# Performance work log

Measured on AMD Instinct MI355X. Metric: run time of the kernel, lower is better.

The kernel has to match this reference:

```python
import math
import jax, jax.numpy as jnp
import numpy as np

B, T, D = 4, 2048, 768
NH, DH = 12, 64

def setup_inputs() -> dict:
    key = jax.random.key(0)
    k1, k2, k3 = jax.random.split(key, 3)
    scale_attn = 1.0 / math.sqrt(D)
    scale_proj = 1.0 / math.sqrt(D)
    return {
        "x": jax.random.normal(k1, (B, T, D), dtype=jnp.float32),
        "w_attn": jax.random.normal(k2, (D, 3 * D), dtype=jnp.float32) * scale_attn,
        "b_attn": jnp.zeros((3 * D,), dtype=jnp.float32),
        "w_proj": jax.random.normal(k3, (D, D), dtype=jnp.float32) * scale_proj,
        "b_proj": jnp.zeros((D,), dtype=jnp.float32),
    }

def reference(x, w_attn, b_attn, w_proj, b_proj):
    Bx, Tx, Dx = x.shape
    qkv = x @ w_attn + b_attn                     # [B, T, 3D]
    q, k, v = jnp.split(qkv, 3, axis=-1)          # each [B, T, D]
    # [B, T, D] -> [B, NH, T, DH]
    def to_heads(t):
        return t.reshape(Bx, Tx, NH, DH).transpose(0, 2, 1, 3)
    q, k, v = to_heads(q), to_heads(k), to_heads(v)
    attn = jnp.einsum("bhqd,bhkd->bhqk", q, k) / math.sqrt(DH)
    causal = jnp.tril(jnp.ones((Tx, Tx), dtype=bool))
    attn = jnp.where(causal[None, None, :, :], attn, -jnp.inf)
    attn = jax.nn.softmax(attn, axis=-1)
    out = jnp.einsum("bhqk,bhkd->bhqd", attn, v)  # [B, NH, T, DH]
    out = out.transpose(0, 2, 1, 3).reshape(Bx, Tx, Dx)
    out = out @ w_proj + b_proj
    return (out, (k, v))
```

## Files before the change

### kernel.cpp

```cpp
#include <hip/hip_runtime.h>
#include <hip/hip_bf16.h>

typedef unsigned short ushort_t;
typedef __attribute__((ext_vector_type(8))) short short8;
typedef __attribute__((ext_vector_type(4))) float f32x4;

#define B_    4
#define T_    2048
#define D_    768
#define NH_   12
#define DH_   64
#define KDIM  768

__device__ __forceinline__ ushort_t f2bf(float f) {
  union { float f; unsigned u; } c; c.f = f;
  unsigned u = c.u;
  return (ushort_t)((u + 0x7FFFu + ((u >> 16) & 1u)) >> 16);
}

__device__ __forceinline__ unsigned cvt_pk_bf16(float lo, float hi) {
  unsigned r;
  asm("v_cvt_pk_bf16_f32 %0, %1, %2" : "=v"(r) : "v"(lo), "v"(hi));
  return r;
}

__device__ __forceinline__ void gload_lds16(const void* g, void* l) {
  __builtin_amdgcn_global_load_lds(
      (const __attribute__((address_space(1))) unsigned int*)g,
      (__attribute__((address_space(3))) unsigned int*)l, 16, 0, 0);
}

__global__ void cvt_bf16_vec(const float* __restrict__ in,
                             ushort_t* __restrict__ out, int n4) {
  int i = blockIdx.x * blockDim.x + threadIdx.x;
  if (i >= n4) return;
  float4 v = ((const float4*)in)[i];
  ushort4 o;
  o.x = f2bf(v.x); o.y = f2bf(v.y); o.z = f2bf(v.z); o.w = f2bf(v.w);
  ((ushort4*)out)[i] = o;
}

__global__ void transpose_cvt(const float* __restrict__ in,
                              ushort_t* __restrict__ out, int R, int C) {
  __shared__ float tile[32][33];
  int c0 = blockIdx.x * 32, r0 = blockIdx.y * 32;
  int tx = threadIdx.x, ty = threadIdx.y;
#pragma unroll
  for (int j = 0; j < 32; j += 8)
    tile[ty + j][tx] = in[(size_t)(r0 + ty + j) * C + c0 + tx];
  __syncthreads();
#pragma unroll
  for (int j = 0; j < 32; j += 8)
    out[(size_t)(c0 + ty + j) * R + r0 + tx] = f2bf(tile[tx][ty + j]);
}

__device__ __forceinline__ void gemm128_mainloop(
    const ushort_t* __restrict__ A, const ushort_t* __restrict__ BT,
    int m0, int n0, ushort_t* lds, f32x4 acc[4][4]) {
  const int t = threadIdx.x;
  const int l = t & 63;
  const int w = t >> 6;
  const int wm = w >> 1, wn = w & 1;
  const int g = l >> 4, qi = l & 15;
  const int c0 = t, c1 = t + 256;
  const int r0 = c0 >> 2, r1 = c1 >> 2;
  const int s0 = (c0 & 3) ^ ((r0 >> 2) & 3);
  const int s1 = (c1 & 3) ^ ((r1 >> 2) & 3);
  const ushort_t* ga0 = A + (size_t)(m0 + r0) * KDIM + (s0 << 3);
  const ushort_t* ga1 = A + (size_t)(m0 + r1) * KDIM + (s1 << 3);
  const ushort_t* gb0 = BT + (size_t)(n0 + r0) * KDIM + (s0 << 3);
  const ushort_t* gb1 = BT + (size_t)(n0 + r1) * KDIM + (s1 << 3);
  const int NK = KDIM / 32;
  const int rsw = (g ^ qi >> 2) << 3;

#pragma unroll
  for (int p = 0; p < 2; ++p) {
    ushort_t* lp = lds + p * 8192;
    int k0 = p * 32;
    gload_lds16(ga0 + k0, lp + w * 512);
    gload_lds16(ga1 + k0, lp + 2048 + w * 512);
    gload_lds16(gb0 + k0, lp + 4096 + w * 512);
    gload_lds16(gb1 + k0, lp + 6144 + w * 512);
  }

  int kb = 0;
  for (int kk = 0; kk < NK; ++kk) {
    if (kk < NK - 1) {
      asm volatile("s_waitcnt vmcnt(4)" ::: "memory");
    } else {
      asm volatile("s_waitcnt vmcnt(0)" ::: "memory");
    }
    __builtin_amdgcn_sched_barrier(0);
    __builtin_amdgcn_s_barrier();
    __builtin_amdgcn_sched_barrier(0);
    if (kk + 2 < NK) {
      int kb2 = kb + 2 >= 3 ? kb - 1 : kb + 2;
      ushort_t* lp = lds + kb2 * 8192;
      int k0 = (kk + 2) * 32;
      gload_lds16(ga0 + k0, lp + w * 512);
      gload_lds16(ga1 + k0, lp + 2048 + w * 512);
      gload_lds16(gb0 + k0, lp + 4096 + w * 512);
      gload_lds16(gb1 + k0, lp + 6144 + w * 512);
    }
    ushort_t* lb = lds + kb * 8192;
    short8 af[4], bfv[4];
#pragma unroll
    for (int mt = 0; mt < 4; ++mt)
      af[mt] = *(const short8*)&lb[(wm * 64 + mt * 16 + qi) * 32 + rsw];
#pragma unroll
    for (int nt = 0; nt < 4; ++nt)
      bfv[nt] = *(const short8*)&lb[4096 + (wn * 64 + nt * 16 + qi) * 32 + rsw];
#pragma unroll
    for (int mt = 0; mt < 4; ++mt)
#pragma unroll
      for (int nt = 0; nt < 4; ++nt)
        acc[mt][nt] = __builtin_amdgcn_mfma_f32_16x16x32_bf16(
            af[mt], bfv[nt], acc[mt][nt], 0, 0, 0);
    kb = kb + 1 >= 3 ? 0 : kb + 1;
  }
}

__global__ __launch_bounds__(256) void gemm_qkv_kernel(
    const ushort_t* __restrict__ xbf, const ushort_t* __restrict__ wT,
    const float* __restrict__ bias, ushort_t* __restrict__ qbf,
    float* __restrict__ kout, float* __restrict__ vout,
    ushort_t* __restrict__ kbf, ushort_t* __restrict__ vtbf) {
  __shared__ ushort_t lds[24576];
  int bid = blockIdx.x;
  int m0 = (bid / 18) << 7;
  int n0 = (bid % 18) << 7;
  f32x4 acc[4][4];
  f32x4 zero = {0.f, 0.f, 0.f, 0.f};
#pragma unroll
  for (int a = 0; a < 4; ++a)
#pragma unroll
    for (int b = 0; b < 4; ++b) acc[a][b] = zero;
  gemm128_mainloop(xbf, wT, m0, n0, lds, acc);

  const float QSC = 0.125f * 1.44269504089f;
  const int l = threadIdx.x & 63, w = threadIdx.x >> 6;
  const int wm = w >> 1, wn = w & 1;
  const int sec = n0 / 768;
  const int b = m0 >> 11;
  const int tt_base = (m0 & 2047) + wm * 64;
#pragma unroll
  for (int nt = 0; nt < 4; ++nt) {
    int n = n0 + wn * 64 + nt * 16 + (l & 15);
    float bv = bias[n];
    int nn = n - sec * 768;
    int h = nn >> 6, dh = nn & 63;
    size_t head_base = ((size_t)(b * NH_ + h) * T_);
#pragma unroll
    for (int mt = 0; mt < 4; ++mt) {
      int tt0 = tt_base + mt * 16 + ((l >> 4) << 2);
      float vals[4];
#pragma unroll
      for (int r = 0; r < 4; ++r) vals[r] = acc[mt][nt][r] + bv;
      if (sec == 0) {
#pragma unroll
        for (int r = 0; r < 4; ++r)
          qbf[((head_base + tt0 + r) << 6) + dh] = f2bf(vals[r] * QSC);
      } else if (sec == 1) {
#pragma unroll
        for (int r = 0; r < 4; ++r) {
          size_t idx = ((head_base + tt0 + r) << 6) + dh;
          kout[idx] = vals[r];
          kbf[idx] = f2bf(vals[r]);
        }
      } else {
#pragma unroll
        for (int r = 0; r < 4; ++r)
          vout[((head_base + tt0 + r) << 6) + dh] = vals[r];
        ushort4 pk;
        pk.x = f2bf(vals[0]); pk.y = f2bf(vals[1]);
        pk.z = f2bf(vals[2]); pk.w = f2bf(vals[3]);
        *(ushort4*)&vtbf[((size_t)(b * NH_ + h) * DH_ + dh) * T_ + tt0] = pk;
      }
    }
  }
}

__global__ __launch_bounds__(256) void gemm_proj_kernel(
    const ushort_t* __restrict__ abf, const ushort_t* __restrict__ wT,
    const float* __restrict__ bias, float* __restrict__ out) {
  __shared__ ushort_t lds[24576];
  int bid = blockIdx.x;
  int m0 = (bid / 6) << 7;
  int n0 = (bid % 6) << 7;
  f32x4 acc[4][4];
  f32x4 zero = {0.f, 0.f, 0.f, 0.f};
#pragma unroll
  for (int a = 0; a < 4; ++a)
#pragma unroll
    for (int b = 0; b < 4; ++b) acc[a][b] = zero;
  gemm128_mainloop(abf, wT, m0, n0, lds, acc);

  const int l = threadIdx.x & 63, w = threadIdx.x >> 6;
  const int wm = w >> 1, wn = w & 1;
#pragma unroll
  for (int nt = 0; nt < 4; ++nt) {
    int n = n0 + wn * 64 + nt * 16 + (l & 15);
    float bv = bias[n];
#pragma unroll
    for (int mt = 0; mt < 4; ++mt) {
#pragma unroll
      for (int r = 0; r < 4; ++r) {
        int m = m0 + wm * 64 + mt * 16 + ((l >> 4) << 2) + r;
        out[(size_t)m * D_ + n] = acc[mt][nt][r] + bv;
      }
    }
  }
}

__device__ __forceinline__ void strip_exp_store(
    f32x4 s4[4], int gq, bool diag, int kvb, int g, int qi, char* pbase) {
  if (diag) {
#pragma unroll
    for (int nt = 0; nt < 4; ++nt)
#pragma unroll
      for (int r = 0; r < 4; ++r) {
        int gk = kvb + nt * 16 + g * 4 + r;
        if (gk > gq) s4[nt][r] = -1e30f;
      }
  }
#pragma unroll
  for (int nt = 0; nt < 4; ++nt) {
    float p0 = exp2f(s4[nt][0]);
    float p1 = exp2f(s4[nt][1]);
    float p2 = exp2f(s4[nt][2]);
    float p3 = exp2f(s4[nt][3]);
    uint2 pk;
    pk.x = cvt_pk_bf16(p0, p1);
    pk.y = cvt_pk_bf16(p2, p3);
    *(uint2*)(pbase + ((nt * 32 + g * 8) ^ ((qi & 7) << 4))) = pk;
  }
}

__global__ __launch_bounds__(512, 6) void attn_fwd_kernel(
    const ushort_t* __restrict__ qbf, const ushort_t* __restrict__ kbf,
    const ushort_t* __restrict__ vtbf, ushort_t* __restrict__ obf) {
  __shared__ ushort_t Kl[2][4096];
  __shared__ ushort_t Vt[2][4096];
  __shared__ ushort_t Pl[8][1024];
  const int bid = blockIdx.x;
  const int swz = (bid & 7) * 96 + (bid >> 3);
  const int jp = swz & 15;
  const int bh = swz >> 4;
  const int qlo = jp << 6, qhi = (31 - jp) << 6;
  const int lastH = 31 - jp, lastL = jp;
  const int t = threadIdx.x, l = t & 63, w = t >> 6;
  const int g = l >> 4, qi = l & 15;
  const bool isHi = (w < 4);
  const int wc = isHi ? w : (w - 4);
  const int qs0 = (isHi ? qhi : qlo) + wc * 16;
  const int lastMe = isHi ? lastH : lastL;

  const ushort_t* Qb = qbf + (size_t)bh * T_ * DH_;
  const ushort_t* Kb = kbf + (size_t)bh * T_ * DH_;
  const ushort_t* Vb = vtbf + (size_t)bh * DH_ * T_;

  const int row0 = t >> 3, ch0 = t & 7;
  const ushort_t* gK0 = Kb + row0 * DH_ + ((ch0 ^ (row0 & 7)) << 3);
  const ushort_t* gV0 = Vb + (size_t)row0 * T_ + ((ch0 ^ (row0 & 7)) << 3);

  short8 aq[2];
  {
    const int qr = qs0 + qi;
    aq[0] = *(const short8*)&Qb[(size_t)qr * DH_ + (g << 3)];
    aq[1] = *(const short8*)&Qb[(size_t)qr * DH_ + (g << 3) + 32];
  }

  short8 ones;
#pragma unroll
  for (int j = 0; j < 8; ++j) ones[j] = (short)0x3F80;

  f32x4 o[4], al;
  f32x4 zero = {0.f, 0.f, 0.f, 0.f};
#pragma unroll
  for (int nt = 0; nt < 4; ++nt) o[nt] = zero;
  al = zero;

  gload_lds16(gK0, &Kl[0][w * 512]);
  gload_lds16(gV0, &Vt[0][w * 512]);

  char* pb = (char*)&Pl[w][0] + qi * 128;

  for (int kt = 0; kt <= lastH; ++kt) {
    const int buf = kt & 1;
    const int kvb = kt << 6;
    asm volatile("s_waitcnt vmcnt(0)" ::: "memory");
    __builtin_amdgcn_sched_barrier(0);
    __builtin_amdgcn_s_barrier();
    __builtin_amdgcn_sched_barrier(0);
    if (kt < lastH) {
      const int nx = kt + 1;
      gload_lds16(gK0 + (size_t)nx * 4096, &Kl[buf ^ 1][w * 512]);
      gload_lds16(gV0 + (size_t)nx * 64, &Vt[buf ^ 1][w * 512]);
    }
    if (kt <= lastMe) {
      f32x4 s4[4];
#pragma unroll
      for (int nt = 0; nt < 4; ++nt) s4[nt] = zero;
#pragma unroll
      for (int h2 = 0; h2 < 2; ++h2) {
#pragma unroll
        for (int nt = 0; nt < 4; ++nt) {
          short8 bk = *(const short8*)&Kl[buf][((nt * 16 + qi) << 6) +
                                              (((g + 4 * h2) ^ (qi & 7)) << 3)];
          s4[nt] = __builtin_amdgcn_mfma_f32_16x16x32_bf16(bk, aq[h2],
                                                           s4[nt], 0, 0, 0);
        }
      }
      strip_exp_store(s4, qs0 + qi, kt == lastMe, kvb, g, qi, pb);
#pragma unroll
      for (int k2 = 0; k2 < 2; ++k2) {
        short8 pf = *(const short8*)(pb + ((g * 16 + k2 * 64) ^ ((qi & 7) << 4)));
#pragma unroll
        for (int nt = 0; nt < 4; ++nt) {
          short8 av = *(const short8*)&Vt[buf][((nt * 16 + qi) << 6) +
                                               (((g + 4 * k2) ^ (qi & 7)) << 3)];
          o[nt] = __builtin_amdgcn_mfma_f32_16x16x32_bf16(av, pf, o[nt],
                                                          0, 0, 0);
        }
        al = __builtin_amdgcn_mfma_f32_16x16x32_bf16(ones, pf, al, 0, 0, 0);
      }
    }
  }

  const int b = bh / NH_, h = bh - b * NH_;
  {
    float inv = 1.f / al[0];
    int q = qs0 + qi;
    size_t rowb = (size_t)(b * T_ + q) * D_ + h * DH_;
#pragma unroll
    for (int nt = 0; nt < 4; ++nt) {
      ushort4 pk;
      pk.x = f2bf(o[nt][0] * inv);
      pk.y = f2bf(o[nt][1] * inv);
      pk.z = f2bf(o[nt][2] * inv);
      pk.w = f2bf(o[nt][3] * inv);
      *(ushort4*)&obf[rowb + nt * 16 + g * 4] = pk;
    }
  }
}

extern "C" void kernel_launch(void* const* d_in, const int* in_sizes, int n_in,
                              void* d_out, int out_size, void* d_ws, size_t ws_size,
                              hipStream_t stream) {
  const float* x      = (const float*)d_in[0];
  const float* w_attn = (const float*)d_in[1];
  const float* b_attn = (const float*)d_in[2];
  const float* w_proj = (const float*)d_in[3];
  const float* b_proj = (const float*)d_in[4];

  float* out  = (float*)d_out;
  float* kout = out + (size_t)B_ * T_ * D_;
  float* vout = kout + (size_t)B_ * T_ * D_;

  char* ws = (char*)d_ws;
  ushort_t* xbf = (ushort_t*)(ws);
  ushort_t* wTa = (ushort_t*)(ws + 12582912);
  ushort_t* wTp = (ushort_t*)(ws + 16121856);
  ushort_t* qbf = (ushort_t*)(ws + 17301504);
  ushort_t* kbf = (ushort_t*)(ws + 29884416);
  ushort_t* vtbf = (ushort_t*)(ws + 42467328);
  ushort_t* abf = xbf;

  cvt_bf16_vec<<<6144, 256, 0, stream>>>(x, xbf, (B_ * T_ * D_) / 4);
  dim3 tb(32, 8);
  transpose_cvt<<<dim3(72, 24), tb, 0, stream>>>(w_attn, wTa, D_, 3 * D_);
  transpose_cvt<<<dim3(24, 24), tb, 0, stream>>>(w_proj, wTp, D_, D_);

  gemm_qkv_kernel<<<64 * 18, 256, 0, stream>>>(xbf, wTa, b_attn, qbf, kout, vout,
                                               kbf, vtbf);
  attn_fwd_kernel<<<768, 512, 0, stream>>>(qbf, kbf, vtbf, abf);
  gemm_proj_kernel<<<64 * 6, 256, 0, stream>>>(abf, wTp, b_proj, out);
}
```

Baseline: 141.8 us.

## Keep softmax probabilities in registers by permuting K rows to match MFMA layout

Drops the per-wave LDS staging buffer for P. K rows are read in a permuted order so the QK^T MFMA output lanes line up with the B-operand layout of the PV MFMA, which lets the exp'd scores be packed to bf16 in registers and fed straight in. The LDS swizzle for K and V is changed to a new XOR pattern to stay conflict-free with the new row mapping. This removes an LDS write/read round trip per tile and frees LDS, which may help occupancy. The cost is more complex index math that must keep the causal mask correct.

```diff
diff --git a/kernel.cpp b/kernel.cpp
--- a/kernel.cpp
+++ b/kernel.cpp
@@ -212,27 +212,30 @@
   }
 }
 
-__device__ __forceinline__ void strip_exp_store(
-    f32x4 s4[4], int gq, bool diag, int kvb, int g, int qi, char* pbase) {
+__device__ __forceinline__ void strip_make_w(
+    f32x4 s4[4], int gq, bool diag, int kvb, int g, short8 w[2]) {
   if (diag) {
 #pragma unroll
-    for (int nt = 0; nt < 4; ++nt)
-#pragma unroll
-      for (int r = 0; r < 4; ++r) {
-        int gk = kvb + nt * 16 + g * 4 + r;
-        if (gk > gq) s4[nt][r] = -1e30f;
-      }
-  }
-#pragma unroll
-  for (int nt = 0; nt < 4; ++nt) {
-    float p0 = exp2f(s4[nt][0]);
-    float p1 = exp2f(s4[nt][1]);
-    float p2 = exp2f(s4[nt][2]);
-    float p3 = exp2f(s4[nt][3]);
-    uint2 pk;
-    pk.x = cvt_pk_bf16(p0, p1);
-    pk.y = cvt_pk_bf16(p2, p3);
-    *(uint2*)(pbase + ((nt * 32 + g * 8) ^ ((qi & 7) << 4))) = pk;
+    for (int nt = 0; nt < 4; ++nt) {
+      int kb0 = kvb + ((nt >> 1) << 5) + (g << 3) + ((nt & 1) << 2);
+#pragma unroll
+      for (int r = 0; r < 4; ++r)
+        if (kb0 + r > gq) s4[nt][r] = -1e30f;
+    }
+  }
+  float p[4][4];
+#pragma unroll
+  for (int nt = 0; nt < 4; ++nt)
+#pragma unroll
+    for (int r = 0; r < 4; ++r) p[nt][r] = exp2f(s4[nt][r]);
+#pragma unroll
+  for (int k2 = 0; k2 < 2; ++k2) {
+    union { unsigned u[4]; short8 s; } c;
+    c.u[0] = cvt_pk_bf16(p[2 * k2][0], p[2 * k2][1]);
+    c.u[1] = cvt_pk_bf16(p[2 * k2][2], p[2 * k2][3]);
+    c.u[2] = cvt_pk_bf16(p[2 * k2 + 1][0], p[2 * k2 + 1][1]);
+    c.u[3] = cvt_pk_bf16(p[2 * k2 + 1][2], p[2 * k2 + 1][3]);
+    w[k2] = c.s;
   }
 }
 
@@ -241,7 +244,6 @@
     const ushort_t* __restrict__ vtbf, ushort_t* __restrict__ obf) {
   __shared__ ushort_t Kl[2][4096];
   __shared__ ushort_t Vt[2][4096];
-  __shared__ ushort_t Pl[8][1024];
   const int bid = blockIdx.x;
   const int swz = (bid & 7) * 96 + (bid >> 3);
   const int jp = swz & 15;
@@ -260,8 +262,9 @@
   const ushort_t* Vb = vtbf + (size_t)bh * DH_ * T_;
 
   const int row0 = t >> 3, ch0 = t & 7;
-  const ushort_t* gK0 = Kb + row0 * DH_ + ((ch0 ^ (row0 & 7)) << 3);
-  const ushort_t* gV0 = Vb + (size_t)row0 * T_ + ((ch0 ^ (row0 & 7)) << 3);
+  const int sw0 = (row0 & 3) | (((row0 >> 3) & 1) << 2);
+  const ushort_t* gK0 = Kb + row0 * DH_ + ((ch0 ^ sw0) << 3);
+  const ushort_t* gV0 = Vb + (size_t)row0 * T_ + ((ch0 ^ sw0) << 3);
 
   short8 aq[2];
   {
@@ -280,10 +283,12 @@
   for (int nt = 0; nt < 4; ++nt) o[nt] = zero;
   al = zero;
 
+  const int swzq = (qi & 3) | (((qi >> 2) & 1) << 2);
+  const int swzv = (qi & 3) | (((qi >> 3) & 1) << 2);
+  const int sigrow = ((qi >> 2) << 3) + (qi & 3);
+
   gload_lds16(gK0, &Kl[0][w * 512]);
   gload_lds16(gV0, &Vt[0][w * 512]);
-
-  char* pb = (char*)&Pl[w][0] + qi * 128;
 
   for (int kt = 0; kt <= lastH; ++kt) {
     const int buf = kt & 1;
@@ -303,26 +308,28 @@
       for (int nt = 0; nt < 4; ++nt) s4[nt] = zero;
 #pragma unroll
       for (int h2 = 0; h2 < 2; ++h2) {
+        const int slotk = ((g + 4 * h2) ^ swzq) << 3;
 #pragma unroll
         for (int nt = 0; nt < 4; ++nt) {
-          short8 bk = *(const short8*)&Kl[buf][((nt * 16 + qi) << 6) +
-                                              (((g + 4 * h2) ^ (qi & 7)) << 3)];
+          int row = ((nt >> 1) << 5) + ((nt & 1) << 2) + sigrow;
+          short8 bk = *(const short8*)&Kl[buf][(row << 6) + slotk];
           s4[nt] = __builtin_amdgcn_mfma_f32_16x16x32_bf16(bk, aq[h2],
                                                            s4[nt], 0, 0, 0);
         }
       }
-      strip_exp_store(s4, qs0 + qi, kt == lastMe, kvb, g, qi, pb);
+      short8 wfr[2];
+      strip_make_w(s4, qs0 + qi, kt == lastMe, kvb, g, wfr);
 #pragma unroll
       for (int k2 = 0; k2 < 2; ++k2) {
-        short8 pf = *(const short8*)(pb + ((g * 16 + k2 * 64) ^ ((qi & 7) << 4)));
+        const int slotv = ((g + 4 * k2) ^ swzv) << 3;
 #pragma unroll
         for (int nt = 0; nt < 4; ++nt) {
-          short8 av = *(const short8*)&Vt[buf][((nt * 16 + qi) << 6) +
-                                               (((g + 4 * k2) ^ (qi & 7)) << 3)];
-          o[nt] = __builtin_amdgcn_mfma_f32_16x16x32_bf16(av, pf, o[nt],
+          short8 av = *(const short8*)&Vt[buf][((nt * 16 + qi) << 6) + slotv];
+          o[nt] = __builtin_amdgcn_mfma_f32_16x16x32_bf16(av, wfr[k2], o[nt],
                                                           0, 0, 0);
         }
-        al = __builtin_amdgcn_mfma_f32_16x16x32_bf16(ones, pf, al, 0, 0, 0);
+        al = __builtin_amdgcn_mfma_f32_16x16x32_bf16(ones, wfr[k2], al,
+                                                     0, 0, 0);
       }
     }
   }
```

Result: faster. 138.9 us (-2.0%).
